# Optimization experiments

Hardware: AMD Instinct MI355X
Metric: run time of the kernel (lower is better)

The kernel has to match this reference:

```python
import jax, jax.numpy as jnp
import numpy as np

B = 8192          # batch
NUM_PROTOS = 10   # num_prototypes
NUM_CLASSES = 10
N_PATCHES = 14 * 14  # 196 non-overlapping 2x2 patches of a 28x28 image


def setup_inputs() -> dict:
    key = jax.random.key(0)
    k1, k2, k3 = jax.random.split(key, 3)
    x = jax.random.normal(k1, (B, 784), dtype=jnp.float32)
    prototypes = jax.random.normal(k2, (NUM_PROTOS, 4), dtype=jnp.float32)
    W = jax.random.normal(k3, (NUM_CLASSES, NUM_PROTOS * N_PATCHES), dtype=jnp.float32) * 0.02
    b = jnp.zeros((NUM_CLASSES,), dtype=jnp.float32)
    return {"x": x, "prototypes": prototypes, "W": W, "b": b}


def _features(x, prototypes):
    # x: (B, 784) -> non-overlapping 2x2 patches, row-major within each patch
    bsz = x.shape[0]
    img = x.reshape(bsz, 28, 28)
    patches = img.reshape(bsz, 14, 2, 14, 2).transpose(0, 1, 3, 2, 4).reshape(bsz, N_PATCHES, 4)
    # Quantum kernel: ansatz applies RY(x_i) then RY(-y_i) per wire on |0000>.
    # |0...0> amplitude factorizes over the 4 wires: prod_i cos((x_i - y_i)/2).
    diff = patches[:, :, None, :] - prototypes[None, None, :, :]   # (B, 196, P, 4)
    kern = jnp.abs(jnp.prod(jnp.cos(0.5 * diff), axis=-1))          # (B, 196, P)
    # torch stacks per-prototype then permutes to (B, P, 196) and flattens
    return kern.transpose(0, 2, 1).reshape(bsz, -1)                 # (B, P*196)


def reference(x, prototypes, W, b):
    feats = _features(x, prototypes)
    logits = feats @ W.T + b
    return jax.nn.log_softmax(logits, axis=-1)
```

## Files before the change

kernel.cpp:

```cpp
#include <hip/hip_runtime.h>
#include <math.h>

#define NPROTO 10
#define NCLS 10
#define NPATCH 196
#define ROW_ELEMS 784
#define WT_STRIDE 12
#define TILE_ROWS 16
#define WT_ELEMS (NPROTO * NPATCH * WT_STRIDE)
#define TABLE_OFF WT_ELEMS

__global__ __launch_bounds__(256) void quanv_prep(
    const float* __restrict__ W, const float* __restrict__ protos,
    float* __restrict__ ws) {
  int idx = blockIdx.x * 256 + threadIdx.x;
  if (idx < WT_ELEMS) {
    int pp = idx / WT_STRIDE;
    int c  = idx - pp * WT_STRIDE;
    ws[idx] = (c < NCLS) ? W[c * (NPROTO * NPATCH) + pp] : 0.0f;
  }
  if (idx < NPROTO * 8) {
    int proto = idx >> 3;
    int j = idx & 7;
    float h = 0.5f * protos[proto * 4 + (j & 3)];
    ws[TABLE_OFF + idx] = (j < 4) ? __cosf(h) : __sinf(h);
  }
}

__global__ __launch_bounds__(256) void quanv_main(
    const float* __restrict__ x, const float* __restrict__ Wt,
    const float* __restrict__ table, const float* __restrict__ bias,
    float* __restrict__ out) {
  __shared__ float lds_x[TILE_ROWS * ROW_ELEMS];

  const int tid = threadIdx.x;
  const int bx  = blockIdx.x;

  const float4* gsrc = (const float4*)(x + (size_t)bx * TILE_ROWS * ROW_ELEMS);
  float4* ldst = (float4*)lds_x;
  #pragma unroll
  for (int i = 0; i < 13; ++i) {
    int idx = tid + i * 256;
    if (idx < TILE_ROWS * ROW_ELEMS / 4) ldst[idx] = gsrc[idx];
  }
  __syncthreads();

  const int wave = tid >> 6;
  const int lane = tid & 63;
  const int rr   = lane >> 4;
  const int p4   = lane & 15;
  const int trow = wave * 4 + rr;
  const float* row = &lds_x[trow * ROW_ELEMS];

  float acc[NCLS];
  #pragma unroll
  for (int c = 0; c < NCLS; ++c) acc[c] = 0.0f;

  for (int it = 0; it < 13; ++it) {
    int p = it * 16 + p4;
    if (p < NPATCH) {
      unsigned up = (unsigned)p;
      int pi = up / 14u;
      int pj = up - pi * 14u;
      int off = pi * 56 + pj * 2;
      float x0 = row[off],      x1 = row[off + 1];
      float x2 = row[off + 28], x3 = row[off + 29];
      float s0 = __sinf(0.5f * x0), c0 = __cosf(0.5f * x0);
      float s1 = __sinf(0.5f * x1), c1 = __cosf(0.5f * x1);
      float s2 = __sinf(0.5f * x2), c2 = __cosf(0.5f * x2);
      float s3 = __sinf(0.5f * x3), c3 = __cosf(0.5f * x3);

      #pragma unroll
      for (int proto = 0; proto < NPROTO; ++proto) {
        const float* tb = table + proto * 8;
        float t0 = c0 * tb[0] + s0 * tb[4];
        float t1 = c1 * tb[1] + s1 * tb[5];
        float t2 = c2 * tb[2] + s2 * tb[6];
        float t3 = c3 * tb[3] + s3 * tb[7];
        float q = fabsf(t0 * t1 * t2 * t3);

        const float* wp = Wt + (size_t)(proto * NPATCH + p) * WT_STRIDE;
        float4 wa = *(const float4*)(wp);
        float4 wb = *(const float4*)(wp + 4);
        float2 wc = *(const float2*)(wp + 8);
        acc[0] += q * wa.x; acc[1] += q * wa.y;
        acc[2] += q * wa.z; acc[3] += q * wa.w;
        acc[4] += q * wb.x; acc[5] += q * wb.y;
        acc[6] += q * wb.z; acc[7] += q * wb.w;
        acc[8] += q * wc.x; acc[9] += q * wc.y;
      }
    }
  }

  #pragma unroll
  for (int c = 0; c < NCLS; ++c) {
    float v = acc[c];
    v += __shfl_xor(v, 1);
    v += __shfl_xor(v, 2);
    v += __shfl_xor(v, 4);
    v += __shfl_xor(v, 8);
    acc[c] = v + bias[c];
  }

  float m = acc[0];
  #pragma unroll
  for (int c = 1; c < NCLS; ++c) m = fmaxf(m, acc[c]);
  float sum = 0.0f;
  #pragma unroll
  for (int c = 0; c < NCLS; ++c) sum += __expf(acc[c] - m);
  float lse = m + __logf(sum);

  if (p4 < NCLS) {
    float v = acc[0];
    #pragma unroll
    for (int c = 1; c < NCLS; ++c) v = (p4 == c) ? acc[c] : v;
    int grow = bx * TILE_ROWS + trow;
    out[grow * NCLS + p4] = v - lse;
  }
}

extern "C" void kernel_launch(void* const* d_in, const int* in_sizes, int n_in,
                              void* d_out, int out_size, void* d_ws, size_t ws_size,
                              hipStream_t stream) {
  const float* x      = (const float*)d_in[0];
  const float* protos = (const float*)d_in[1];
  const float* W      = (const float*)d_in[2];
  const float* bias   = (const float*)d_in[3];
  float* out = (float*)d_out;
  float* ws  = (float*)d_ws;

  quanv_prep<<<(WT_ELEMS + 255) / 256, 256, 0, stream>>>(W, protos, ws);
  quanv_main<<<8192 / TILE_ROWS, 256, 0, stream>>>(x, ws, ws + TABLE_OFF, bias, out);
}
```

Baseline: 100.6 us.

## Split work by image row across blocks with atomic reduction and separate softmax

Rather than staging 16 full rows in LDS per block, each block now handles 64 batch rows for one of the 14 patch rows, and lanes read x straight from global memory. Partial logits are reduced through LDS atomics and then global atomicAdd into the output. A third kernel applies bias and log-softmax afterward. Weights are re-laid out as [patch][proto][class] so the loads are wave-uniform. The aim is more parallelism and fewer LDS loads, paid for with global atomics, an extra launch, and uncoalesced strided reads of x.

Measured after the change: 108.8 us. 8.2% more time.

```diff
diff --git a/kernel.cpp b/kernel.cpp
--- a/kernel.cpp
+++ b/kernel.cpp
@@ -1,122 +1,116 @@
 #include <hip/hip_runtime.h>
 #include <math.h>
 
+#define B_ROWS 8192
 #define NPROTO 10
 #define NCLS 10
 #define NPATCH 196
-#define ROW_ELEMS 784
-#define WT_STRIDE 12
-#define TILE_ROWS 16
-#define WT_ELEMS (NPROTO * NPATCH * WT_STRIDE)
-#define TABLE_OFF WT_ELEMS
+
+#define TABLE_OFF 0
+#define WT2_OFF   80
+#define WT2_ELEMS (NPATCH * NPROTO * NCLS)
+#define WS_NEEDED ((size_t)(WT2_OFF + WT2_ELEMS) * sizeof(float))
 
 __global__ __launch_bounds__(256) void quanv_prep(
     const float* __restrict__ W, const float* __restrict__ protos,
-    float* __restrict__ ws) {
+    float* __restrict__ ws, float* __restrict__ out, int buildWt2) {
   int idx = blockIdx.x * 256 + threadIdx.x;
-  if (idx < WT_ELEMS) {
-    int pp = idx / WT_STRIDE;
-    int c  = idx - pp * WT_STRIDE;
-    ws[idx] = (c < NCLS) ? W[c * (NPROTO * NPATCH) + pp] : 0.0f;
-  }
   if (idx < NPROTO * 8) {
     int proto = idx >> 3;
     int j = idx & 7;
     float h = 0.5f * protos[proto * 4 + (j & 3)];
     ws[TABLE_OFF + idx] = (j < 4) ? __cosf(h) : __sinf(h);
   }
+  if (buildWt2 && idx < WT2_ELEMS) {
+    int p     = idx / (NPROTO * NCLS);
+    int rem   = idx - p * (NPROTO * NCLS);
+    int proto = rem / NCLS;
+    int c     = rem - proto * NCLS;
+    ws[WT2_OFF + idx] = W[c * (NPROTO * NPATCH) + proto * NPATCH + p];
+  }
+  if (idx < B_ROWS * NCLS) out[idx] = 0.0f;
 }
 
+template <bool USE_WT2>
 __global__ __launch_bounds__(256) void quanv_main(
-    const float* __restrict__ x, const float* __restrict__ Wt,
-    const float* __restrict__ table, const float* __restrict__ bias,
-    float* __restrict__ out) {
-  __shared__ float lds_x[TILE_ROWS * ROW_ELEMS];
+    const float* __restrict__ x, const float* __restrict__ ws,
+    const float* __restrict__ W, float* __restrict__ out) {
+  __shared__ float red[64 * NCLS];
 
   const int tid = threadIdx.x;
-  const int bx  = blockIdx.x;
-
-  const float4* gsrc = (const float4*)(x + (size_t)bx * TILE_ROWS * ROW_ELEMS);
-  float4* ldst = (float4*)lds_x;
-  #pragma unroll
-  for (int i = 0; i < 13; ++i) {
-    int idx = tid + i * 256;
-    if (idx < TILE_ROWS * ROW_ELEMS / 4) ldst[idx] = gsrc[idx];
-  }
+  for (int i = tid; i < 64 * NCLS; i += 256) red[i] = 0.0f;
   __syncthreads();
 
-  const int wave = tid >> 6;
+  const int wid  = __builtin_amdgcn_readfirstlane(tid >> 6);
   const int lane = tid & 63;
-  const int rr   = lane >> 4;
-  const int p4   = lane & 15;
-  const int trow = wave * 4 + rr;
-  const float* row = &lds_x[trow * ROW_ELEMS];
+  const int r    = blockIdx.x * 64 + lane;
+  const int pr   = blockIdx.y;
+
+  const float* tb  = ws + TABLE_OFF;
+  const float* Wt2 = ws + WT2_OFF;
+
+  const int pj0 = (wid < 2) ? wid * 4 : 8 + (wid - 2) * 3;
+  const int npj = (wid < 2) ? 4 : 3;
 
   float acc[NCLS];
-  #pragma unroll
+#pragma unroll
   for (int c = 0; c < NCLS; ++c) acc[c] = 0.0f;
 
-  for (int it = 0; it < 13; ++it) {
-    int p = it * 16 + p4;
-    if (p < NPATCH) {
-      unsigned up = (unsigned)p;
-      int pi = up / 14u;
-      int pj = up - pi * 14u;
-      int off = pi * 56 + pj * 2;
-      float x0 = row[off],      x1 = row[off + 1];
-      float x2 = row[off + 28], x3 = row[off + 29];
-      float s0 = __sinf(0.5f * x0), c0 = __cosf(0.5f * x0);
-      float s1 = __sinf(0.5f * x1), c1 = __cosf(0.5f * x1);
-      float s2 = __sinf(0.5f * x2), c2 = __cosf(0.5f * x2);
-      float s3 = __sinf(0.5f * x3), c3 = __cosf(0.5f * x3);
+  const float* xr = x + (size_t)r * 784 + pr * 56;
 
-      #pragma unroll
-      for (int proto = 0; proto < NPROTO; ++proto) {
-        const float* tb = table + proto * 8;
-        float t0 = c0 * tb[0] + s0 * tb[4];
-        float t1 = c1 * tb[1] + s1 * tb[5];
-        float t2 = c2 * tb[2] + s2 * tb[6];
-        float t3 = c3 * tb[3] + s3 * tb[7];
-        float q = fabsf(t0 * t1 * t2 * t3);
+  for (int j = 0; j < npj; ++j) {
+    int pj = pj0 + j;
+    int p  = pr * 14 + pj;
+    float2 a01 = *(const float2*)(xr + 2 * pj);
+    float2 a23 = *(const float2*)(xr + 2 * pj + 28);
+    float s0, c0, s1, c1, s2, c2, s3, c3;
+    __sincosf(0.5f * a01.x, &s0, &c0);
+    __sincosf(0.5f * a01.y, &s1, &c1);
+    __sincosf(0.5f * a23.x, &s2, &c2);
+    __sincosf(0.5f * a23.y, &s3, &c3);
 
-        const float* wp = Wt + (size_t)(proto * NPATCH + p) * WT_STRIDE;
-        float4 wa = *(const float4*)(wp);
-        float4 wb = *(const float4*)(wp + 4);
-        float2 wc = *(const float2*)(wp + 8);
-        acc[0] += q * wa.x; acc[1] += q * wa.y;
-        acc[2] += q * wa.z; acc[3] += q * wa.w;
-        acc[4] += q * wb.x; acc[5] += q * wb.y;
-        acc[6] += q * wb.z; acc[7] += q * wb.w;
-        acc[8] += q * wc.x; acc[9] += q * wc.y;
+#pragma unroll
+    for (int proto = 0; proto < NPROTO; ++proto) {
+      const float* t8 = tb + proto * 8;
+      float t0 = fmaf(c0, t8[0], s0 * t8[4]);
+      float t1 = fmaf(c1, t8[1], s1 * t8[5]);
+      float t2 = fmaf(c2, t8[2], s2 * t8[6]);
+      float t3 = fmaf(c3, t8[3], s3 * t8[7]);
+      float q  = fabsf((t0 * t1) * (t2 * t3));
+#pragma unroll
+      for (int c = 0; c < NCLS; ++c) {
+        float w = USE_WT2 ? Wt2[p * (NPROTO * NCLS) + proto * NCLS + c]
+                          : W[c * (NPROTO * NPATCH) + proto * NPATCH + p];
+        acc[c] = fmaf(q, w, acc[c]);
       }
     }
   }
 
-  #pragma unroll
+#pragma unroll
+  for (int c = 0; c < NCLS; ++c) atomicAdd(&red[lane * NCLS + c], acc[c]);
+  __syncthreads();
+
+  for (int i = tid; i < 64 * NCLS; i += 256) {
+    atomicAdd(&out[(size_t)blockIdx.x * 64 * NCLS + i], red[i]);
+  }
+}
+
+__global__ __launch_bounds__(256) void quanv_softmax(
+    float* __restrict__ out, const float* __restrict__ bias) {
+  int r = blockIdx.x * 256 + threadIdx.x;
+  float v[NCLS];
+  float m = -1e30f;
+#pragma unroll
   for (int c = 0; c < NCLS; ++c) {
-    float v = acc[c];
-    v += __shfl_xor(v, 1);
-    v += __shfl_xor(v, 2);
-    v += __shfl_xor(v, 4);
-    v += __shfl_xor(v, 8);
-    acc[c] = v + bias[c];
+    v[c] = out[r * NCLS + c] + bias[c];
+    m = fmaxf(m, v[c]);
   }
-
-  float m = acc[0];
-  #pragma unroll
-  for (int c = 1; c < NCLS; ++c) m = fmaxf(m, acc[c]);
   float sum = 0.0f;
-  #pragma unroll
-  for (int c = 0; c < NCLS; ++c) sum += __expf(acc[c] - m);
+#pragma unroll
+  for (int c = 0; c < NCLS; ++c) sum += __expf(v[c] - m);
   float lse = m + __logf(sum);
-
-  if (p4 < NCLS) {
-    float v = acc[0];
-    #pragma unroll
-    for (int c = 1; c < NCLS; ++c) v = (p4 == c) ? acc[c] : v;
-    int grow = bx * TILE_ROWS + trow;
-    out[grow * NCLS + p4] = v - lse;
-  }
+#pragma unroll
+  for (int c = 0; c < NCLS; ++c) out[r * NCLS + c] = v[c] - lse;
 }
 
 extern "C" void kernel_launch(void* const* d_in, const int* in_sizes, int n_in,
@@ -129,6 +123,15 @@
   float* out = (float*)d_out;
   float* ws  = (float*)d_ws;
 
-  quanv_prep<<<(WT_ELEMS + 255) / 256, 256, 0, stream>>>(W, protos, ws);
-  quanv_main<<<8192 / TILE_ROWS, 256, 0, stream>>>(x, ws, ws + TABLE_OFF, bias, out);
+  const bool useWt2 = (ws_size >= WS_NEEDED);
+
+  quanv_prep<<<(B_ROWS * NCLS + 255) / 256, 256, 0, stream>>>(W, protos, ws, out, useWt2 ? 1 : 0);
+
+  dim3 grid(B_ROWS / 64, 14);
+  if (useWt2)
+    quanv_main<true><<<grid, 256, 0, stream>>>(x, ws, W, out);
+  else
+    quanv_main<false><<<grid, 256, 0, stream>>>(x, ws, W, out);
+
+  quanv_softmax<<<B_ROWS / 256, 256, 0, stream>>>(out, bias);
 }
```
